# Kernel tuning notes

Measured on AMD Instinct MI355X. Metric: run time of the kernel, lower is better.

Reference implementation:

```python
import jax, jax.numpy as jnp
import numpy as np

NUM_ITER = 20
EPS = 1e-8


def _conv(x, w, pad):
    # x: [N, Cin, H, W], w: [Cout, Cin, kh, kw] (cross-correlation, like torch conv2d)
    return jax.lax.conv_general_dilated(
        x, w, window_strides=(1, 1), padding=pad,
        dimension_numbers=('NCHW', 'OIHW', 'NCHW'))


def setup_inputs() -> dict:
    key = jax.random.key(0)
    x = jax.random.normal(key, (2, 4, 3, 256, 256), dtype=jnp.float32)
    return {
        'x': x,
        'lam': jnp.array([0.02], dtype=jnp.float32),
        'tau': jnp.array([0.25], dtype=jnp.float32),
        'theta': jnp.array([0.1], dtype=jnp.float32),
        'wx': jnp.array([[-1.0, 1.0, 0.0]], dtype=jnp.float32),
        'wy': jnp.array([[-1.0], [1.0], [0.0]], dtype=jnp.float32),
    }


def reference(x, lam, tau, theta, wx, wy):
    # x: [2, B, C, H, W] -> pairs of single-channel images [NB, 2, H, W]
    F, B, C, H, W = x.shape
    NB = B * C
    xx = jnp.moveaxis(x.reshape(2, NB, H, W), 0, 1)  # [NB, 2, H, W]

    dt = x.dtype
    gx = jnp.array([[-1., 0., 1.], [-2., 0., 2.], [-1., 0., 1.]], dt) / 6.0
    gy = jnp.array([[-1., -2., -1.], [0., 0., 0.], [1., 2., 1.]], dt) / 6.0
    grad_w = jnp.stack([gx, gy])[:, None]          # [2,1,3,3] image gradient (fixed)
    gxu = jnp.array([[0., 0., 0.], [0., -1., 1.], [0., 0., 0.]], dt)
    gyu = jnp.array([[0., 0., 0.], [0., -1., 0.], [0., 1., 0.]], dt)
    grad_u_w = jnp.stack([gxu, gyu])[:, None]      # [2,1,3,3] flow gradient (fixed)
    wx_k = wx[None, None]                          # [1,1,1,3] trainable divergence stencil
    wy_k = wy[None, None]                          # [1,1,3,1]

    rho_c = (xx[:, 1] - xx[:, 0])[:, None]                       # [NB,1,H,W]
    grad_im = _conv(xx[:, 1:], grad_w, [(1, 1), (1, 1)])         # [NB,2,H,W]
    norm_grad = jnp.sum(grad_im * grad_im, axis=1, keepdims=True) + EPS

    u = jnp.zeros((NB, 2, H, W), dt)
    p1 = jnp.zeros((NB, 2, H, W), dt)
    p2 = jnp.zeros((NB, 2, H, W), dt)

    tl = theta * lam       # [1]
    tt = tau / theta       # [1]

    def div(p):  # p: [NB,2,H,W] -> [NB,1,H,W]
        return (_conv(p[:, 0:1], wx_k, [(0, 0), (1, 1)]) +
                _conv(p[:, 1:2], wy_k, [(1, 1), (0, 0)]))

    def body(carry, _):
        u, p1, p2 = carry
        rho = rho_c + jnp.sum(grad_im * u, axis=1, keepdims=True)
        th = tl * norm_grad
        v = u - jnp.where(jnp.abs(rho) < th,
                          rho * grad_im / norm_grad,
                          tl * grad_im * jnp.sign(rho))
        u0 = v[:, 0] + theta * div(p1)[:, 0]
        u1 = v[:, 1] + theta * div(p2)[:, 0]
        u = jnp.stack([u0, u1], axis=1)
        g1 = _conv(u[:, 0:1], grad_u_w, [(1, 1), (1, 1)])
        g2 = _conv(u[:, 1:2], grad_u_w, [(1, 1), (1, 1)])
        p1 = (p1 + tt * g1) / (1.0 + tt * jnp.sum(jnp.abs(g1), axis=1, keepdims=True))
        p2 = (p2 + tt * g2) / (1.0 + tt * jnp.sum(jnp.abs(g2), axis=1, keepdims=True))
        return (u, p1, p2), None

    (u, p1, p2), _ = jax.lax.scan(body, (u, p1, p2), None, length=NUM_ITER)
    return u.reshape(B, C, 2, H, W)
```

## Files before the change

kernel.cpp:

```cpp
#include <hip/hip_runtime.h>

#define W 256
#define H 256
#define HW (W*H)
#define NB 12
#define ROWS 16
#define BPI (H/ROWS)
#define NBLK (NB*BPI)
#define NTHREADS 1024
#define NUM_ITER 20
#define TVEPS 1e-8f
#define HPLANES 8
#define FLAG_MAGIC 0x5A170000


__device__ __forceinline__ float aload(const float* p) {
    return __hip_atomic_load(p, __ATOMIC_RELAXED, __HIP_MEMORY_SCOPE_AGENT);
}
__device__ __forceinline__ void astore(float* p, float v) {
    __hip_atomic_store(p, v, __ATOMIC_RELAXED, __HIP_MEMORY_SCOPE_AGENT);
}
__device__ __forceinline__ void waitflag(const int* f, int tgt) {
    while (__hip_atomic_load(f, __ATOMIC_RELAXED, __HIP_MEMORY_SCOPE_AGENT) != tgt)
        __builtin_amdgcn_s_sleep(1);
    asm volatile("" ::: "memory");
}
__device__ __forceinline__ void setflag(int* f, int tgt) {
    asm volatile("s_waitcnt vmcnt(0)" ::: "memory");
    __hip_atomic_store(f, tgt, __ATOMIC_RELAXED, __HIP_MEMORY_SCOPE_AGENT);
}
__device__ __forceinline__ float fastrcp(float x) { return __builtin_amdgcn_rcpf(x); }

#define LD4(dst, ptr) { const float4 _t = *reinterpret_cast<const float4*>(ptr); \
                        dst[0]=_t.x; dst[1]=_t.y; dst[2]=_t.z; dst[3]=_t.w; }
#define ST4(ptr, src) { float4 _t; _t.x=src[0]; _t.y=src[1]; _t.z=src[2]; _t.w=src[3]; \
                        *reinterpret_cast<float4*>(ptr) = _t; }

__global__ __launch_bounds__(NTHREADS, 1) void tvl1_ovl_kernel(
    const float* __restrict__ xin,
    const float* __restrict__ lam,
    const float* __restrict__ tau,
    const float* __restrict__ theta,
    const float* __restrict__ wxv,
    const float* __restrict__ wyv,
    float* __restrict__ uout,
    float* __restrict__ halo,
    int* __restrict__ flags)
{
    __shared__ float xu0[ROWS+1][W];
    __shared__ float xu1[ROWS+1][W];
    __shared__ float xq1[ROWS][W];
    __shared__ float xq2[ROWS][W];

    const int tid  = threadIdx.x;
    const int lane = tid & 63;
    const int wv   = tid >> 6;
    const int x0   = lane << 2;
    const int b    = blockIdx.x;
    const int n    = b / BPI, bi = b % BPI;
    const int r0   = bi * ROWS;
    const int grow = r0 + wv;
    const bool notTop = (bi > 0), notBot = (bi < BPI-1);

    const float th0 = theta[0];
    const float tl  = th0 * lam[0];
    const float tt  = tau[0] / th0;
    const float wx0 = wxv[0], wx1 = wxv[1], wx2 = wxv[2];
    const float wy0 = wyv[0], wy1 = wyv[1], wy2 = wyv[2];

    const float* __restrict__ I0 = xin + (size_t)n * HW;
    const float* __restrict__ I1 = xin + (size_t)(NB + n) * HW;

    auto grad4 = [&](int row, float* rr, float* ggx, float* ggy) {
        #pragma unroll
        for (int c = 0; c < 4; ++c) {
            const int xc = x0 + c;
            const int idx = row * W + xc;
            const bool xm = xc > 0, xp = xc < W-1, ym = row > 0, yp = row < H-1;
            float a00=0.f,a01=0.f,a02=0.f,a10=0.f,a12=0.f,a20=0.f,a21=0.f,a22=0.f;
            if (ym) { a01=I1[idx-W]; if (xm) a00=I1[idx-W-1]; if (xp) a02=I1[idx-W+1]; }
            if (xm) a10=I1[idx-1];
            if (xp) a12=I1[idx+1];
            if (yp) { a21=I1[idx+W]; if (xm) a20=I1[idx+W-1]; if (xp) a22=I1[idx+W+1]; }
            ggx[c] = ((a02-a00) + 2.f*(a12-a10) + (a22-a20)) * (1.f/6.f);
            ggy[c] = ((a20-a00) + 2.f*(a21-a01) + (a22-a02)) * (1.f/6.f);
            rr[c]  = I1[idx] - I0[idx];
        }
    };

    float rho[4], gxr[4], gyr[4];
    grad4(grow, rho, gxr, gyr);
    float rho16[4]={0,0,0,0}, gx16[4]={0,0,0,0}, gy16[4]={0,0,0,0};
    if (wv == 14 && notBot) grad4(r0 + ROWS, rho16, gx16, gy16);

    for (int k = tid; k < (ROWS+1)*W; k += NTHREADS) { (&xu0[0][0])[k]=0.f; (&xu1[0][0])[k]=0.f; }
    for (int k = tid; k < ROWS*W;     k += NTHREADS) { (&xq1[0][0])[k]=0.f; (&xq2[0][0])[k]=0.f; }
    float u0[4]={0,0,0,0}, u1[4]={0,0,0,0};
    float p1x[4]={0,0,0,0}, p1y[4]={0,0,0,0}, p2x[4]={0,0,0,0}, p2y[4]={0,0,0,0};
    __syncthreads();

    auto ustep_dym = [&](const float* rr, const float* ggx, const float* ggy,
                         const float* uu0, const float* uu1,
                         const float* x1, const float* q1c, const float* q1p,
                         const float* x2, const float* q2c, const float* q2p,
                         float* o0, float* o1) {
        float l1 = __shfl_up(x1[3],1), l2 = __shfl_up(x2[3],1);
        if (lane == 0) { l1 = 0.f; l2 = 0.f; }
        float r1 = __shfl_down(x1[0],1), r2 = __shfl_down(x2[0],1);
        if (lane == 63) { r1 = 0.f; r2 = 0.f; }
        const float x1m[4]={l1,x1[0],x1[1],x1[2]}, x1p[4]={x1[1],x1[2],x1[3],r1};
        const float x2m[4]={l2,x2[0],x2[1],x2[2]}, x2p[4]={x2[1],x2[2],x2[3],r2};
        #pragma unroll
        for (int c = 0; c < 4; ++c) {
            const float r  = rr[c] + ggx[c]*uu0[c] + ggy[c]*uu1[c];
            const float ng = ggx[c]*ggx[c] + ggy[c]*ggy[c] + TVEPS;
            const float f  = (fabsf(r) < tl*ng) ? (r * fastrcp(ng)) : copysignf(tl, r);
            const float d1 = wx0*x1m[c] + wx1*x1[c] + wx2*x1p[c] + wy1*q1c[c] + wy2*q1p[c];
            const float d2 = wx0*x2m[c] + wx1*x2[c] + wx2*x2p[c] + wy1*q2c[c] + wy2*q2p[c];
            o0[c] = (uu0[c] - f*ggx[c]) + th0*d1;
            o1[c] = (uu1[c] - f*ggy[c]) + th0*d2;
        }
    };
    auto ustep_dyp = [&](const float* rr, const float* ggx, const float* ggy,
                         const float* uu0, const float* uu1,
                         const float* x1, const float* q1m, const float* q1c,
                         const float* x2, const float* q2m, const float* q2c,
                         float* o0, float* o1) {
        float l1 = __shfl_up(x1[3],1), l2 = __shfl_up(x2[3],1);
        if (lane == 0) { l1 = 0.f; l2 = 0.f; }
        float r1 = __shfl_down(x1[0],1), r2 = __shfl_down(x2[0],1);
        if (lane == 63) { r1 = 0.f; r2 = 0.f; }
        const float x1m[4]={l1,x1[0],x1[1],x1[2]}, x1p[4]={x1[1],x1[2],x1[3],r1};
        const float x2m[4]={l2,x2[0],x2[1],x2[2]}, x2p[4]={x2[1],x2[2],x2[3],r2};
        #pragma unroll
        for (int c = 0; c < 4; ++c) {
            const float r  = rr[c] + ggx[c]*uu0[c] + ggy[c]*uu1[c];
            const float ng = ggx[c]*ggx[c] + ggy[c]*ggy[c] + TVEPS;
            const float f  = (fabsf(r) < tl*ng) ? (r * fastrcp(ng)) : copysignf(tl, r);
            const float d1 = wx0*x1m[c] + wx1*x1[c] + wx2*x1p[c] + wy0*q1m[c] + wy1*q1c[c];
            const float d2 = wx0*x2m[c] + wx1*x2[c] + wx2*x2p[c] + wy0*q2m[c] + wy1*q2c[c];
            o0[c] = (uu0[c] - f*ggx[c]) + th0*d1;
            o1[c] = (uu1[c] - f*ggy[c]) + th0*d2;
        }
    };
    auto ustepF = [&](const float* q1m, const float* q1p, const float* q2m, const float* q2p) {
        float l1 = __shfl_up(p1x[3],1), l2 = __shfl_up(p2x[3],1);
        if (lane == 0) { l1 = 0.f; l2 = 0.f; }
        float r1 = __shfl_down(p1x[0],1), r2 = __shfl_down(p2x[0],1);
        if (lane == 63) { r1 = 0.f; r2 = 0.f; }
        const float x1m[4]={l1,p1x[0],p1x[1],p1x[2]}, x1p[4]={p1x[1],p1x[2],p1x[3],r1};
        const float x2m[4]={l2,p2x[0],p2x[1],p2x[2]}, x2p[4]={p2x[1],p2x[2],p2x[3],r2};
        #pragma unroll
        for (int c = 0; c < 4; ++c) {
            const float r  = rho[c] + gxr[c]*u0[c] + gyr[c]*u1[c];
            const float ng = gxr[c]*gxr[c] + gyr[c]*gyr[c] + TVEPS;
            const float f  = (fabsf(r) < tl*ng) ? (r * fastrcp(ng)) : copysignf(tl, r);
            const float d1 = wx0*x1m[c] + wx1*p1x[c] + wx2*x1p[c]
                           + wy0*q1m[c] + wy1*p1y[c] + wy2*q1p[c];
            const float d2 = wx0*x2m[c] + wx1*p2x[c] + wx2*x2p[c]
                           + wy0*q2m[c] + wy1*p2y[c] + wy2*q2p[c];
            u0[c] = (u0[c] - f*gxr[c]) + th0*d1;
            u1[c] = (u1[c] - f*gyr[c]) + th0*d2;
        }
    };

    for (int it = 0; it < NUM_ITER; ++it) {
        const bool last = (it == NUM_ITER-1);

        if (wv == 0) {
            float pyp1[4], pyp2[4];
            LD4(pyp1, &xq1[1][x0]); LD4(pyp2, &xq2[1][x0]);
            float o0[4], o1[4];
            ustep_dym(rho, gxr, gyr, u0, u1, p1x, p1y, pyp1, p2x, p2y, pyp2, o0, o1);
            float hym1[4]={0,0,0,0}, hym2[4]={0,0,0,0};
            if (it > 0 && notTop) {
                if (lane == 0) waitflag(&flags[(size_t)(it-1)*3*NBLK + 2*NBLK + (b-1)],
                                        FLAG_MAGIC | (it-1));
                const float* hp = halo + ((size_t)(it-1)*NBLK + (b-1))*HPLANES*W;
                #pragma unroll
                for (int c = 0; c < 4; ++c) {
                    hym1[c] = aload(hp + 6*W + x0 + c);
                    hym2[c] = aload(hp + 7*W + x0 + c);
                }
            }
            #pragma unroll
            for (int c = 0; c < 4; ++c) {
                u0[c] = o0[c] + th0*(wy0*hym1[c]);
                u1[c] = o1[c] + th0*(wy0*hym2[c]);
            }
        } else if (wv == ROWS-1) {
            float pym1[4], pym2[4];
            LD4(pym1, &xq1[ROWS-2][x0]); LD4(pym2, &xq2[ROWS-2][x0]);
            float o0[4], o1[4];
            ustep_dyp(rho, gxr, gyr, u0, u1, p1x, pym1, p1y, p2x, pym2, p2y, o0, o1);
            float hyp1[4]={0,0,0,0}, hyp2[4]={0,0,0,0};
            if (it > 0 && notBot) {
                if (lane == 0) waitflag(&flags[(size_t)(it-1)*3*NBLK + 0*NBLK + (b+1)],
                                        FLAG_MAGIC | (it-1));
                const float* hp = halo + ((size_t)(it-1)*NBLK + (b+1))*HPLANES*W;
                #pragma unroll
                for (int c = 0; c < 4; ++c) {
                    hyp1[c] = aload(hp + 1*W + x0 + c);
                    hyp2[c] = aload(hp + 3*W + x0 + c);
                }
            }
            #pragma unroll
            for (int c = 0; c < 4; ++c) {
                u0[c] = o0[c] + th0*(wy2*hyp1[c]);
                u1[c] = o1[c] + th0*(wy2*hyp2[c]);
            }
        } else {
            float pym1[4], pym2[4], pyp1[4], pyp2[4];
            LD4(pym1, &xq1[wv-1][x0]); LD4(pym2, &xq2[wv-1][x0]);
            LD4(pyp1, &xq1[wv+1][x0]); LD4(pyp2, &xq2[wv+1][x0]);
            ustepF(pym1, pyp1, pym2, pyp2);
        }

        if (last) {
            float* __restrict__ o0 = uout + (size_t)(2*n)   * HW + (size_t)grow * W + x0;
            float* __restrict__ o1 = uout + (size_t)(2*n+1) * HW + (size_t)grow * W + x0;
            ST4(o0, u0); ST4(o1, u1);
            break;
        }
        ST4(&xu0[wv][x0], u0); ST4(&xu1[wv][x0], u1);

        if (wv == 14 && notBot) {
            float c16x1[4]={0,0,0,0}, c16x2[4]={0,0,0,0};
            float c16c1[4]={0,0,0,0}, c16c2[4]={0,0,0,0};
            float c16p1[4]={0,0,0,0}, c16p2[4]={0,0,0,0};
            if (it > 0) {
                int* fb = flags + (size_t)(it-1)*3*NBLK;
                if (lane < 2) waitflag(&fb[lane*NBLK + (b+1)], FLAG_MAGIC | (it-1));
                const float* hp = halo + ((size_t)(it-1)*NBLK + (b+1))*HPLANES*W;
                #pragma unroll
                for (int c = 0; c < 4; ++c) {
                    c16x1[c] = aload(hp + 0*W + x0 + c);
                    c16c1[c] = aload(hp + 1*W + x0 + c);
                    c16x2[c] = aload(hp + 2*W + x0 + c);
                    c16c2[c] = aload(hp + 3*W + x0 + c);
                    c16p1[c] = aload(hp + 4*W + x0 + c);
                    c16p2[c] = aload(hp + 5*W + x0 + c);
                }
            }
            float q115[4], q215[4], u160[4], u161[4];
            LD4(q115, &xq1[ROWS-1][x0]); LD4(q215, &xq2[ROWS-1][x0]);
            LD4(u160, &xu0[ROWS][x0]);   LD4(u161, &xu1[ROWS][x0]);
            float n160[4], n161[4];
            ustep_dym(rho16, gx16, gy16, u160, u161,
                      c16x1, c16c1, c16p1, c16x2, c16c2, c16p2, n160, n161);
            #pragma unroll
            for (int c = 0; c < 4; ++c) {
                n160[c] += th0*(wy0*q115[c]);
                n161[c] += th0*(wy0*q215[c]);
            }
            ST4(&xu0[ROWS][x0], n160); ST4(&xu1[ROWS][x0], n161);
        }
        __syncthreads();

        float uy0[4], uy1[4];
        if (grow == H-1) { for (int c=0;c<4;++c){ uy0[c]=0.f; uy1[c]=0.f; } }
        else             { LD4(uy0, &xu0[wv+1][x0]); LD4(uy1, &xu1[wv+1][x0]); }
        float ur0 = __shfl_down(u0[0], 1), ur1 = __shfl_down(u1[0], 1);
        if (lane == 63) { ur0 = 0.f; ur1 = 0.f; }
        #pragma unroll
        for (int c = 0; c < 4; ++c) {
            const float uxp0 = (c < 3) ? u0[c+1] : ur0;
            const float uxp1 = (c < 3) ? u1[c+1] : ur1;
            const float g1x = uxp0 - u0[c];
            const float g1y = uy0[c] - u0[c];
            const float g2x = uxp1 - u1[c];
            const float g2y = uy1[c] - u1[c];
            const float rc1 = fastrcp(1.f + tt * (fabsf(g1x) + fabsf(g1y)));
            const float rc2 = fastrcp(1.f + tt * (fabsf(g2x) + fabsf(g2y)));
            p1x[c] = (p1x[c] + tt*g1x) * rc1;
            p1y[c] = (p1y[c] + tt*g1y) * rc1;
            p2x[c] = (p2x[c] + tt*g2x) * rc2;
            p2y[c] = (p2y[c] + tt*g2y) * rc2;
        }
        ST4(&xq1[wv][x0], p1y); ST4(&xq2[wv][x0], p2y);

        {
            float* hw = halo + ((size_t)it * NBLK + b) * HPLANES * W;
            int* fw = flags + (size_t)it * 3 * NBLK;
            const int ft = FLAG_MAGIC | it;
            if (wv == 0 && notTop) {
                #pragma unroll
                for (int c = 0; c < 4; ++c) {
                    astore(hw + 0*W + x0 + c, p1x[c]);
                    astore(hw + 1*W + x0 + c, p1y[c]);
                    astore(hw + 2*W + x0 + c, p2x[c]);
                    astore(hw + 3*W + x0 + c, p2y[c]);
                }
                if (lane == 0) setflag(&fw[0*NBLK + b], ft);
            } else if (wv == 1 && notTop) {
                #pragma unroll
                for (int c = 0; c < 4; ++c) {
                    astore(hw + 4*W + x0 + c, p1y[c]);
                    astore(hw + 5*W + x0 + c, p2y[c]);
                }
                if (lane == 0) setflag(&fw[1*NBLK + b], ft);
            } else if (wv == ROWS-1 && notBot) {
                #pragma unroll
                for (int c = 0; c < 4; ++c) {
                    astore(hw + 6*W + x0 + c, p1y[c]);
                    astore(hw + 7*W + x0 + c, p2y[c]);
                }
                if (lane == 0) setflag(&fw[2*NBLK + b], ft);
            }
        }
        __syncthreads();
    }
}


__global__ void precompute_kernel(const float* __restrict__ x,
                                  float* __restrict__ u,
                                  float* __restrict__ ws) {
    const int row = blockIdx.x;
    const int n = row / H, y = row % H;
    const int xx = threadIdx.x;
    const int idx = y * W + xx;
    const float* __restrict__ I0 = x + (size_t)n * HW;
    const float* __restrict__ I1 = x + (size_t)(NB + n) * HW;
    float* __restrict__ p1  = ws;
    float* __restrict__ p2  = ws + (size_t)2 * NB * HW;
    float* __restrict__ rho = ws + (size_t)4 * NB * HW;
    float* __restrict__ gxp = ws + (size_t)5 * NB * HW;
    float* __restrict__ gyp = ws + (size_t)6 * NB * HW;
    const float i1c = I1[idx];
    const bool xm = xx > 0, xp = xx < W - 1, ym = y > 0, yp = y < H - 1;
    float a00=0.f,a01=0.f,a02=0.f,a10=0.f,a12=0.f,a20=0.f,a21=0.f,a22=0.f;
    if (ym) { a01 = I1[idx-W]; if (xm) a00 = I1[idx-W-1]; if (xp) a02 = I1[idx-W+1]; }
    if (xm) a10 = I1[idx-1];
    if (xp) a12 = I1[idx+1];
    if (yp) { a21 = I1[idx+W]; if (xm) a20 = I1[idx+W-1]; if (xp) a22 = I1[idx+W+1]; }
    const float gxv = ((a02-a00) + 2.f*(a12-a10) + (a22-a20)) * (1.f/6.f);
    const float gyv = ((a20-a00) + 2.f*(a21-a01) + (a22-a02)) * (1.f/6.f);
    const size_t np = (size_t)n * HW;
    rho[np+idx] = i1c - I0[idx];
    gxp[np+idx] = gxv;
    gyp[np+idx] = gyv;
    u[(size_t)(2*n)*HW + idx] = 0.f;   u[(size_t)(2*n+1)*HW + idx] = 0.f;
    p1[(size_t)(2*n)*HW + idx] = 0.f;  p1[(size_t)(2*n+1)*HW + idx] = 0.f;
    p2[(size_t)(2*n)*HW + idx] = 0.f;  p2[(size_t)(2*n+1)*HW + idx] = 0.f;
}

__global__ void u_kernel(const float* __restrict__ ws,
                         float* __restrict__ u,
                         const float* __restrict__ lam,
                         const float* __restrict__ theta,
                         const float* __restrict__ wxv,
                         const float* __restrict__ wyv) {
    const int row = blockIdx.x;
    const int n = row / H, y = row % H;
    const int xx = threadIdx.x;
    const int idx = y * W + xx;
    const size_t np = (size_t)n * HW;
    const float* __restrict__ p1  = ws;
    const float* __restrict__ p2  = ws + (size_t)2 * NB * HW;
    const float* __restrict__ rho_c = ws + (size_t)4 * NB * HW;
    const float* __restrict__ gxp = ws + (size_t)5 * NB * HW;
    const float* __restrict__ gyp = ws + (size_t)6 * NB * HW;
    const float th0 = theta[0];
    const float tl = th0 * lam[0];
    const float wx0 = wxv[0], wx1 = wxv[1], wx2 = wxv[2];
    const float wy0 = wyv[0], wy1 = wyv[1], wy2 = wyv[2];
    const float gx = gxp[np+idx];
    const float gy = gyp[np+idx];
    float* __restrict__ u0p = u + (size_t)(2*n)*HW;
    float* __restrict__ u1p = u + (size_t)(2*n+1)*HW;
    const float u0 = u0p[idx], u1 = u1p[idx];
    const float rho = rho_c[np+idx] + gx*u0 + gy*u1;
    const float ng = gx*gx + gy*gy + TVEPS;
    const float th = tl * ng;
    float s0, s1;
    if (fabsf(rho) < th) { const float d = rho/ng; s0 = d*gx; s1 = d*gy; }
    else { const float sg = (rho > 0.f) ? 1.f : ((rho < 0.f) ? -1.f : 0.f);
           s0 = tl*gx*sg; s1 = tl*gy*sg; }
    const float v0 = u0 - s0, v1 = u1 - s1;
    const float* __restrict__ p1xp = p1 + (size_t)(2*n)*HW;
    const float* __restrict__ p1yp = p1 + (size_t)(2*n+1)*HW;
    const float* __restrict__ p2xp = p2 + (size_t)(2*n)*HW;
    const float* __restrict__ p2yp = p2 + (size_t)(2*n+1)*HW;
    float d1 = wx1*p1xp[idx] + wy1*p1yp[idx];
    float d2 = wx1*p2xp[idx] + wy1*p2yp[idx];
    if (xx > 0)     { d1 += wx0*p1xp[idx-1]; d2 += wx0*p2xp[idx-1]; }
    if (xx < W-1)   { d1 += wx2*p1xp[idx+1]; d2 += wx2*p2xp[idx+1]; }
    if (y > 0)      { d1 += wy0*p1yp[idx-W]; d2 += wy0*p2yp[idx-W]; }
    if (y < H-1)    { d1 += wy2*p1yp[idx+W]; d2 += wy2*p2yp[idx+W]; }
    u0p[idx] = v0 + th0*d1;
    u1p[idx] = v1 + th0*d2;
}

__global__ void p_kernel(const float* __restrict__ u,
                         float* __restrict__ ws,
                         const float* __restrict__ tau,
                         const float* __restrict__ theta) {
    const int row = blockIdx.x;
    const int n = row / H, y = row % H;
    const int xx = threadIdx.x;
    const int idx = y * W + xx;
    float* __restrict__ p1 = ws;
    float* __restrict__ p2 = ws + (size_t)2 * NB * HW;
    const float tt = tau[0] / theta[0];
    const float* __restrict__ u0p = u + (size_t)(2*n)*HW;
    const float* __restrict__ u1p = u + (size_t)(2*n+1)*HW;
    const float c0 = u0p[idx];
    const float g1x = ((xx < W-1) ? u0p[idx+1] : 0.f) - c0;
    const float g1y = ((y < H-1) ? u0p[idx+W] : 0.f) - c0;
    const float c1 = u1p[idx];
    const float g2x = ((xx < W-1) ? u1p[idx+1] : 0.f) - c1;
    const float g2y = ((y < H-1) ? u1p[idx+W] : 0.f) - c1;
    float* __restrict__ p1xp = p1 + (size_t)(2*n)*HW;
    float* __restrict__ p1yp = p1 + (size_t)(2*n+1)*HW;
    float* __restrict__ p2xp = p2 + (size_t)(2*n)*HW;
    float* __restrict__ p2yp = p2 + (size_t)(2*n+1)*HW;
    const float den1 = 1.f + tt * (fabsf(g1x) + fabsf(g1y));
    p1xp[idx] = (p1xp[idx] + tt*g1x) / den1;
    p1yp[idx] = (p1yp[idx] + tt*g1y) / den1;
    const float den2 = 1.f + tt * (fabsf(g2x) + fabsf(g2y));
    p2xp[idx] = (p2xp[idx] + tt*g2x) / den2;
    p2yp[idx] = (p2yp[idx] + tt*g2y) / den2;
}

extern "C" void kernel_launch(void* const* d_in, const int* in_sizes, int n_in,
                              void* d_out, int out_size, void* d_ws, size_t ws_size,
                              hipStream_t stream) {
    const float* x     = (const float*)d_in[0];
    const float* lam   = (const float*)d_in[1];
    const float* tau   = (const float*)d_in[2];
    const float* theta = (const float*)d_in[3];
    const float* wxv   = (const float*)d_in[4];
    const float* wyv   = (const float*)d_in[5];
    float* u = (float*)d_out;

    const size_t halo_floats = (size_t)(NUM_ITER-1) * NBLK * HPLANES * W;
    const size_t need = halo_floats * sizeof(float)
                      + (size_t)(NUM_ITER-1) * 3 * NBLK * sizeof(int);

    if (ws_size >= need) {
        float* halo = (float*)d_ws;
        int* flags = (int*)((char*)d_ws + halo_floats * sizeof(float));
        void* args[] = { (void*)&x, (void*)&lam, (void*)&tau, (void*)&theta,
                         (void*)&wxv, (void*)&wyv, (void*)&u, (void*)&halo, (void*)&flags };
        hipLaunchCooperativeKernel((void*)tvl1_ovl_kernel, dim3(NBLK), dim3(NTHREADS),
                                   args, 0, stream);
    } else {
        float* ws = (float*)d_ws;
        const dim3 grid(NB * H);
        const dim3 block(W);
        precompute_kernel<<<grid, block, 0, stream>>>(x, u, ws);
        for (int it = 0; it < NUM_ITER; ++it) {
            u_kernel<<<grid, block, 0, stream>>>(ws, u, lam, theta, wxv, wyv);
            p_kernel<<<grid, block, 0, stream>>>(u, ws, tau, theta);
        }
    }
}
```

Baseline: 111.3 us.

## Defer cross-block halo waits past local u-step and use LDS flags for boundary rows

Restructures each iteration so boundary waves run their local u-update first and only wait on neighbour halo data after the workgroup barrier, folding the halo contribution in later. Flag stores for the previous iteration's halo are deferred to the start of the next iteration so the memory waitcnt overlaps other work. Wave 14 keeps its recomputed ghost row in registers and exchanges boundary rows with wave 15 through LDS flags instead of an extra barrier. This aims to hide inter-block spin-wait latency, at the cost of more complex ordering and possible subtle sync bugs.

```diff
diff --git a/kernel.cpp b/kernel.cpp
--- a/kernel.cpp
+++ b/kernel.cpp
@@ -29,6 +29,12 @@
     asm volatile("s_waitcnt vmcnt(0)" ::: "memory");
     __hip_atomic_store(f, tgt, __ATOMIC_RELAXED, __HIP_MEMORY_SCOPE_AGENT);
 }
+__device__ __forceinline__ void lset(int* f, int v) {
+    __hip_atomic_store(f, v, __ATOMIC_RELEASE, __HIP_MEMORY_SCOPE_WORKGROUP);
+}
+__device__ __forceinline__ void lwait(int* f, int v) {
+    while (__hip_atomic_load(f, __ATOMIC_ACQUIRE, __HIP_MEMORY_SCOPE_WORKGROUP) < v) {}
+}
 __device__ __forceinline__ float fastrcp(float x) { return __builtin_amdgcn_rcpf(x); }
 
 #define LD4(dst, ptr) { const float4 _t = *reinterpret_cast<const float4*>(ptr); \
@@ -36,7 +42,7 @@
 #define ST4(ptr, src) { float4 _t; _t.x=src[0]; _t.y=src[1]; _t.z=src[2]; _t.w=src[3]; \
                         *reinterpret_cast<float4*>(ptr) = _t; }
 
-__global__ __launch_bounds__(NTHREADS, 1) void tvl1_ovl_kernel(
+__global__ __launch_bounds__(NTHREADS, 1) void tvl1_pb_kernel(
     const float* __restrict__ xin,
     const float* __restrict__ lam,
     const float* __restrict__ tau,
@@ -51,6 +57,7 @@
     __shared__ float xu1[ROWS+1][W];
     __shared__ float xq1[ROWS][W];
     __shared__ float xq2[ROWS][W];
+    __shared__ int   sF[2];
 
     const int tid  = threadIdx.x;
     const int lane = tid & 63;
@@ -91,10 +98,12 @@
     float rho[4], gxr[4], gyr[4];
     grad4(grow, rho, gxr, gyr);
     float rho16[4]={0,0,0,0}, gx16[4]={0,0,0,0}, gy16[4]={0,0,0,0};
+    float u16_0[4]={0,0,0,0}, u16_1[4]={0,0,0,0};
     if (wv == 14 && notBot) grad4(r0 + ROWS, rho16, gx16, gy16);
 
     for (int k = tid; k < (ROWS+1)*W; k += NTHREADS) { (&xu0[0][0])[k]=0.f; (&xu1[0][0])[k]=0.f; }
     for (int k = tid; k < ROWS*W;     k += NTHREADS) { (&xq1[0][0])[k]=0.f; (&xq2[0][0])[k]=0.f; }
+    if (tid == 0) { sF[0] = 0; sF[1] = 0; }
     float u0[4]={0,0,0,0}, u1[4]={0,0,0,0};
     float p1x[4]={0,0,0,0}, p1y[4]={0,0,0,0}, p2x[4]={0,0,0,0}, p2y[4]={0,0,0,0};
     __syncthreads();
@@ -163,113 +172,15 @@
             u1[c] = (u1[c] - f*gyr[c]) + th0*d2;
         }
     };
-
-    for (int it = 0; it < NUM_ITER; ++it) {
-        const bool last = (it == NUM_ITER-1);
-
-        if (wv == 0) {
-            float pyp1[4], pyp2[4];
-            LD4(pyp1, &xq1[1][x0]); LD4(pyp2, &xq2[1][x0]);
-            float o0[4], o1[4];
-            ustep_dym(rho, gxr, gyr, u0, u1, p1x, p1y, pyp1, p2x, p2y, pyp2, o0, o1);
-            float hym1[4]={0,0,0,0}, hym2[4]={0,0,0,0};
-            if (it > 0 && notTop) {
-                if (lane == 0) waitflag(&flags[(size_t)(it-1)*3*NBLK + 2*NBLK + (b-1)],
-                                        FLAG_MAGIC | (it-1));
-                const float* hp = halo + ((size_t)(it-1)*NBLK + (b-1))*HPLANES*W;
-                #pragma unroll
-                for (int c = 0; c < 4; ++c) {
-                    hym1[c] = aload(hp + 6*W + x0 + c);
-                    hym2[c] = aload(hp + 7*W + x0 + c);
-                }
-            }
-            #pragma unroll
-            for (int c = 0; c < 4; ++c) {
-                u0[c] = o0[c] + th0*(wy0*hym1[c]);
-                u1[c] = o1[c] + th0*(wy0*hym2[c]);
-            }
-        } else if (wv == ROWS-1) {
-            float pym1[4], pym2[4];
-            LD4(pym1, &xq1[ROWS-2][x0]); LD4(pym2, &xq2[ROWS-2][x0]);
-            float o0[4], o1[4];
-            ustep_dyp(rho, gxr, gyr, u0, u1, p1x, pym1, p1y, p2x, pym2, p2y, o0, o1);
-            float hyp1[4]={0,0,0,0}, hyp2[4]={0,0,0,0};
-            if (it > 0 && notBot) {
-                if (lane == 0) waitflag(&flags[(size_t)(it-1)*3*NBLK + 0*NBLK + (b+1)],
-                                        FLAG_MAGIC | (it-1));
-                const float* hp = halo + ((size_t)(it-1)*NBLK + (b+1))*HPLANES*W;
-                #pragma unroll
-                for (int c = 0; c < 4; ++c) {
-                    hyp1[c] = aload(hp + 1*W + x0 + c);
-                    hyp2[c] = aload(hp + 3*W + x0 + c);
-                }
-            }
-            #pragma unroll
-            for (int c = 0; c < 4; ++c) {
-                u0[c] = o0[c] + th0*(wy2*hyp1[c]);
-                u1[c] = o1[c] + th0*(wy2*hyp2[c]);
-            }
-        } else {
-            float pym1[4], pym2[4], pyp1[4], pyp2[4];
-            LD4(pym1, &xq1[wv-1][x0]); LD4(pym2, &xq2[wv-1][x0]);
-            LD4(pyp1, &xq1[wv+1][x0]); LD4(pyp2, &xq2[wv+1][x0]);
-            ustepF(pym1, pyp1, pym2, pyp2);
-        }
-
-        if (last) {
-            float* __restrict__ o0 = uout + (size_t)(2*n)   * HW + (size_t)grow * W + x0;
-            float* __restrict__ o1 = uout + (size_t)(2*n+1) * HW + (size_t)grow * W + x0;
-            ST4(o0, u0); ST4(o1, u1);
-            break;
-        }
-        ST4(&xu0[wv][x0], u0); ST4(&xu1[wv][x0], u1);
-
-        if (wv == 14 && notBot) {
-            float c16x1[4]={0,0,0,0}, c16x2[4]={0,0,0,0};
-            float c16c1[4]={0,0,0,0}, c16c2[4]={0,0,0,0};
-            float c16p1[4]={0,0,0,0}, c16p2[4]={0,0,0,0};
-            if (it > 0) {
-                int* fb = flags + (size_t)(it-1)*3*NBLK;
-                if (lane < 2) waitflag(&fb[lane*NBLK + (b+1)], FLAG_MAGIC | (it-1));
-                const float* hp = halo + ((size_t)(it-1)*NBLK + (b+1))*HPLANES*W;
-                #pragma unroll
-                for (int c = 0; c < 4; ++c) {
-                    c16x1[c] = aload(hp + 0*W + x0 + c);
-                    c16c1[c] = aload(hp + 1*W + x0 + c);
-                    c16x2[c] = aload(hp + 2*W + x0 + c);
-                    c16c2[c] = aload(hp + 3*W + x0 + c);
-                    c16p1[c] = aload(hp + 4*W + x0 + c);
-                    c16p2[c] = aload(hp + 5*W + x0 + c);
-                }
-            }
-            float q115[4], q215[4], u160[4], u161[4];
-            LD4(q115, &xq1[ROWS-1][x0]); LD4(q215, &xq2[ROWS-1][x0]);
-            LD4(u160, &xu0[ROWS][x0]);   LD4(u161, &xu1[ROWS][x0]);
-            float n160[4], n161[4];
-            ustep_dym(rho16, gx16, gy16, u160, u161,
-                      c16x1, c16c1, c16p1, c16x2, c16c2, c16p2, n160, n161);
-            #pragma unroll
-            for (int c = 0; c < 4; ++c) {
-                n160[c] += th0*(wy0*q115[c]);
-                n161[c] += th0*(wy0*q215[c]);
-            }
-            ST4(&xu0[ROWS][x0], n160); ST4(&xu1[ROWS][x0], n161);
-        }
-        __syncthreads();
-
-        float uy0[4], uy1[4];
-        if (grow == H-1) { for (int c=0;c<4;++c){ uy0[c]=0.f; uy1[c]=0.f; } }
-        else             { LD4(uy0, &xu0[wv+1][x0]); LD4(uy1, &xu1[wv+1][x0]); }
-        float ur0 = __shfl_down(u0[0], 1), ur1 = __shfl_down(u1[0], 1);
+    auto pstep = [&](const float* uy0, const float* uy1) {
+        float ur0 = __shfl_down(u0[0],1), ur1 = __shfl_down(u1[0],1);
         if (lane == 63) { ur0 = 0.f; ur1 = 0.f; }
         #pragma unroll
         for (int c = 0; c < 4; ++c) {
             const float uxp0 = (c < 3) ? u0[c+1] : ur0;
             const float uxp1 = (c < 3) ? u1[c+1] : ur1;
-            const float g1x = uxp0 - u0[c];
-            const float g1y = uy0[c] - u0[c];
-            const float g2x = uxp1 - u1[c];
-            const float g2y = uy1[c] - u1[c];
+            const float g1x = uxp0 - u0[c], g1y = uy0[c] - u0[c];
+            const float g2x = uxp1 - u1[c], g2y = uy1[c] - u1[c];
             const float rc1 = fastrcp(1.f + tt * (fabsf(g1x) + fabsf(g1y)));
             const float rc2 = fastrcp(1.f + tt * (fabsf(g2x) + fabsf(g2y)));
             p1x[c] = (p1x[c] + tt*g1x) * rc1;
@@ -277,13 +188,115 @@
             p2x[c] = (p2x[c] + tt*g2x) * rc2;
             p2y[c] = (p2y[c] + tt*g2y) * rc2;
         }
-        ST4(&xq1[wv][x0], p1y); ST4(&xq2[wv][x0], p2y);
-
-        {
-            float* hw = halo + ((size_t)it * NBLK + b) * HPLANES * W;
-            int* fw = flags + (size_t)it * 3 * NBLK;
-            const int ft = FLAG_MAGIC | it;
-            if (wv == 0 && notTop) {
+    };
+
+    for (int it = 0; it < NUM_ITER; ++it) {
+        const bool last = (it == NUM_ITER-1);
+        const int fseq = it + 1;
+
+        if (it > 0 && lane == 0) {
+            int* fw = flags + (size_t)(it-1) * 3 * NBLK;
+            const int ft = FLAG_MAGIC | (it-1);
+            if (wv == 0 && notTop)           setflag(&fw[0*NBLK + b], ft);
+            else if (wv == 1 && notTop)      setflag(&fw[1*NBLK + b], ft);
+            else if (wv == ROWS-1 && notBot) setflag(&fw[2*NBLK + b], ft);
+        }
+
+        if (wv == 0) {
+            float pyp1v[4], pyp2v[4];
+            LD4(pyp1v, &xq1[1][x0]); LD4(pyp2v, &xq2[1][x0]);
+            float o0[4], o1[4];
+            ustep_dym(rho, gxr, gyr, u0, u1, p1x, p1y, pyp1v, p2x, p2y, pyp2v, o0, o1);
+            if (last) {
+                float hym1[4]={0,0,0,0}, hym2[4]={0,0,0,0};
+                if (it > 0 && notTop) {
+                    if (lane == 0) waitflag(&flags[(size_t)(it-1)*3*NBLK + 2*NBLK + (b-1)],
+                                            FLAG_MAGIC | (it-1));
+                    const float* hp = halo + ((size_t)(it-1)*NBLK + (b-1))*HPLANES*W;
+                    #pragma unroll
+                    for (int c = 0; c < 4; ++c) {
+                        hym1[c] = aload(hp + 6*W + x0 + c);
+                        hym2[c] = aload(hp + 7*W + x0 + c);
+                    }
+                }
+                #pragma unroll
+                for (int c = 0; c < 4; ++c) {
+                    u0[c] = o0[c] + th0*(wy0*hym1[c]);
+                    u1[c] = o1[c] + th0*(wy0*hym2[c]);
+                }
+            } else {
+                #pragma unroll
+                for (int c = 0; c < 4; ++c) { u0[c] = o0[c]; u1[c] = o1[c]; }
+            }
+        } else if (wv == ROWS-1) {
+            float pym1v[4], pym2v[4];
+            LD4(pym1v, &xq1[ROWS-2][x0]); LD4(pym2v, &xq2[ROWS-2][x0]);
+            float o0[4], o1[4];
+            ustep_dyp(rho, gxr, gyr, u0, u1, p1x, pym1v, p1y, p2x, pym2v, p2y, o0, o1);
+            if (last) {
+                float hyp1[4]={0,0,0,0}, hyp2[4]={0,0,0,0};
+                if (it > 0 && notBot) {
+                    if (lane == 0) waitflag(&flags[(size_t)(it-1)*3*NBLK + 0*NBLK + (b+1)],
+                                            FLAG_MAGIC | (it-1));
+                    const float* hp = halo + ((size_t)(it-1)*NBLK + (b+1))*HPLANES*W;
+                    #pragma unroll
+                    for (int c = 0; c < 4; ++c) {
+                        hyp1[c] = aload(hp + 1*W + x0 + c);
+                        hyp2[c] = aload(hp + 3*W + x0 + c);
+                    }
+                }
+                #pragma unroll
+                for (int c = 0; c < 4; ++c) {
+                    u0[c] = o0[c] + th0*(wy2*hyp1[c]);
+                    u1[c] = o1[c] + th0*(wy2*hyp2[c]);
+                }
+            } else {
+                #pragma unroll
+                for (int c = 0; c < 4; ++c) { u0[c] = o0[c]; u1[c] = o1[c]; }
+            }
+        } else {
+            float pym1v[4], pym2v[4], pyp1v[4], pyp2v[4];
+            LD4(pym1v, &xq1[wv-1][x0]); LD4(pym2v, &xq2[wv-1][x0]);
+            LD4(pyp1v, &xq1[wv+1][x0]); LD4(pyp2v, &xq2[wv+1][x0]);
+            ustepF(pym1v, pyp1v, pym2v, pyp2v);
+        }
+        float q115[4], q215[4];
+        if (wv == 14 && notBot && !last) {
+            LD4(q115, &xq1[ROWS-1][x0]); LD4(q215, &xq2[ROWS-1][x0]);
+        }
+
+        if (last) {
+            float* __restrict__ o0p = uout + (size_t)(2*n)   * HW + (size_t)grow * W + x0;
+            float* __restrict__ o1p = uout + (size_t)(2*n+1) * HW + (size_t)grow * W + x0;
+            ST4(o0p, u0); ST4(o1p, u1);
+            break;
+        }
+        if (wv >= 1 && wv <= 14) { ST4(&xu0[wv][x0], u0); ST4(&xu1[wv][x0], u1); }
+        __syncthreads();
+
+        if (wv == 0) {
+            float hym1[4]={0,0,0,0}, hym2[4]={0,0,0,0};
+            if (it > 0 && notTop) {
+                if (lane == 0) waitflag(&flags[(size_t)(it-1)*3*NBLK + 2*NBLK + (b-1)],
+                                        FLAG_MAGIC | (it-1));
+                const float* hp = halo + ((size_t)(it-1)*NBLK + (b-1))*HPLANES*W;
+                #pragma unroll
+                for (int c = 0; c < 4; ++c) {
+                    hym1[c] = aload(hp + 6*W + x0 + c);
+                    hym2[c] = aload(hp + 7*W + x0 + c);
+                }
+            }
+            #pragma unroll
+            for (int c = 0; c < 4; ++c) {
+                u0[c] += th0*(wy0*hym1[c]);
+                u1[c] += th0*(wy0*hym2[c]);
+            }
+            float uy0[4], uy1[4];
+            LD4(uy0, &xu0[1][x0]); LD4(uy1, &xu1[1][x0]);
+            pstep(uy0, uy1);
+            ST4(&xq1[0][x0], p1y); ST4(&xq2[0][x0], p2y);
+            if (notTop) {
+                float* hw = halo + ((size_t)it * NBLK + b) * HPLANES * W;
                 #pragma unroll
                 for (int c = 0; c < 4; ++c) {
                     astore(hw + 0*W + x0 + c, p1x[c]);
@@ -291,21 +304,85 @@
                     astore(hw + 2*W + x0 + c, p2x[c]);
                     astore(hw + 3*W + x0 + c, p2y[c]);
                 }
-                if (lane == 0) setflag(&fw[0*NBLK + b], ft);
-            } else if (wv == 1 && notTop) {
+            }
+        } else if (wv == ROWS-1) {
+            float hyp1[4]={0,0,0,0}, hyp2[4]={0,0,0,0};
+            if (it > 0 && notBot) {
+                if (lane == 0) waitflag(&flags[(size_t)(it-1)*3*NBLK + 0*NBLK + (b+1)],
+                                        FLAG_MAGIC | (it-1));
+                const float* hp = halo + ((size_t)(it-1)*NBLK + (b+1))*HPLANES*W;
+                #pragma unroll
+                for (int c = 0; c < 4; ++c) {
+                    hyp1[c] = aload(hp + 1*W + x0 + c);
+                    hyp2[c] = aload(hp + 3*W + x0 + c);
+                }
+            }
+            #pragma unroll
+            for (int c = 0; c < 4; ++c) {
+                u0[c] += th0*(wy2*hyp1[c]);
+                u1[c] += th0*(wy2*hyp2[c]);
+            }
+            ST4(&xu0[ROWS-1][x0], u0); ST4(&xu1[ROWS-1][x0], u1);
+            lset(&sF[0], fseq);
+            float uy0[4], uy1[4];
+            if (grow == H-1) { for (int c=0;c<4;++c){ uy0[c]=0.f; uy1[c]=0.f; } }
+            else { lwait(&sF[1], fseq); LD4(uy0, &xu0[ROWS][x0]); LD4(uy1, &xu1[ROWS][x0]); }
+            pstep(uy0, uy1);
+            ST4(&xq1[ROWS-1][x0], p1y); ST4(&xq2[ROWS-1][x0], p2y);
+            if (notBot) {
+                float* hw = halo + ((size_t)it * NBLK + b) * HPLANES * W;
+                #pragma unroll
+                for (int c = 0; c < 4; ++c) {
+                    astore(hw + 6*W + x0 + c, p1y[c]);
+                    astore(hw + 7*W + x0 + c, p2y[c]);
+                }
+            }
+        } else if (wv == 14) {
+            if (notBot) {
+                float pl0[4]={0,0,0,0}, pl1[4]={0,0,0,0}, pl2[4]={0,0,0,0};
+                float pl3[4]={0,0,0,0}, pl4[4]={0,0,0,0}, pl5[4]={0,0,0,0};
+                if (it > 0) {
+                    int* fb = flags + (size_t)(it-1)*3*NBLK;
+                    if (lane < 2) waitflag(&fb[lane*NBLK + (b+1)], FLAG_MAGIC | (it-1));
+                    const float* hp = halo + ((size_t)(it-1)*NBLK + (b+1))*HPLANES*W;
+                    #pragma unroll
+                    for (int c = 0; c < 4; ++c) {
+                        pl0[c] = aload(hp + 0*W + x0 + c);
+                        pl1[c] = aload(hp + 1*W + x0 + c);
+                        pl2[c] = aload(hp + 2*W + x0 + c);
+                        pl3[c] = aload(hp + 3*W + x0 + c);
+                        pl4[c] = aload(hp + 4*W + x0 + c);
+                        pl5[c] = aload(hp + 5*W + x0 + c);
+                    }
+                }
+                float n0[4], n1[4];
+                ustep_dym(rho16, gx16, gy16, u16_0, u16_1,
+                          pl0, pl1, pl4, pl2, pl3, pl5, n0, n1);
+                #pragma unroll
+                for (int c = 0; c < 4; ++c) {
+                    u16_0[c] = n0[c] + th0*(wy0*q115[c]);
+                    u16_1[c] = n1[c] + th0*(wy0*q215[c]);
+                }
+                ST4(&xu0[ROWS][x0], u16_0); ST4(&xu1[ROWS][x0], u16_1);
+                lset(&sF[1], fseq);
+            }
+            lwait(&sF[0], fseq);
+            float uy0[4], uy1[4];
+            LD4(uy0, &xu0[ROWS-1][x0]); LD4(uy1, &xu1[ROWS-1][x0]);
+            pstep(uy0, uy1);
+            ST4(&xq1[14][x0], p1y); ST4(&xq2[14][x0], p2y);
+        } else {
+            float uy0[4], uy1[4];
+            LD4(uy0, &xu0[wv+1][x0]); LD4(uy1, &xu1[wv+1][x0]);
+            pstep(uy0, uy1);
+            ST4(&xq1[wv][x0], p1y); ST4(&xq2[wv][x0], p2y);
+            if (wv == 1 && notTop) {
+                float* hw = halo + ((size_t)it * NBLK + b) * HPLANES * W;
                 #pragma unroll
                 for (int c = 0; c < 4; ++c) {
                     astore(hw + 4*W + x0 + c, p1y[c]);
                     astore(hw + 5*W + x0 + c, p2y[c]);
                 }
-                if (lane == 0) setflag(&fw[1*NBLK + b], ft);
-            } else if (wv == ROWS-1 && notBot) {
-                #pragma unroll
-                for (int c = 0; c < 4; ++c) {
-                    astore(hw + 6*W + x0 + c, p1y[c]);
-                    astore(hw + 7*W + x0 + c, p2y[c]);
-                }
-                if (lane == 0) setflag(&fw[2*NBLK + b], ft);
             }
         }
         __syncthreads();
@@ -443,7 +520,7 @@
         int* flags = (int*)((char*)d_ws + halo_floats * sizeof(float));
         void* args[] = { (void*)&x, (void*)&lam, (void*)&tau, (void*)&theta,
                          (void*)&wxv, (void*)&wyv, (void*)&u, (void*)&halo, (void*)&flags };
-        hipLaunchCooperativeKernel((void*)tvl1_ovl_kernel, dim3(NBLK), dim3(NTHREADS),
+        hipLaunchCooperativeKernel((void*)tvl1_pb_kernel, dim3(NBLK), dim3(NTHREADS),
                                    args, 0, stream);
     } else {
         float* ws = (float*)d_ws;
```

Result: slower. 119.8 us (+7.6%).

## Defer halo flag publication past barrier and opportunistically prefetch neighbor halos

Applied to the files above, without the earlier changes.

Halo-ready flags are no longer set right after the halo stores. They are set at the start of the next iteration, after the block barrier, which removes the vmcnt(0) drain from the critical path before __syncthreads. Boundary waves now peek at the neighbor's flag before their own u-step. If it is already set, they load the halo rows early to overlap latency, and they fall back to the blocking wait only when it is not. The risk is that flag publication is delayed by up to one barrier, which could lengthen neighbors' waits, and correctness relies on relaxed atomic ordering.

```diff
diff --git a/kernel.cpp b/kernel.cpp
--- a/kernel.cpp
+++ b/kernel.cpp
@@ -25,6 +25,9 @@
         __builtin_amdgcn_s_sleep(1);
     asm volatile("" ::: "memory");
 }
+__device__ __forceinline__ int peekflag(const int* f) {
+    return __hip_atomic_load(f, __ATOMIC_RELAXED, __HIP_MEMORY_SCOPE_AGENT);
+}
 __device__ __forceinline__ void setflag(int* f, int tgt) {
     asm volatile("s_waitcnt vmcnt(0)" ::: "memory");
     __hip_atomic_store(f, tgt, __ATOMIC_RELAXED, __HIP_MEMORY_SCOPE_AGENT);
@@ -36,7 +39,7 @@
 #define ST4(ptr, src) { float4 _t; _t.x=src[0]; _t.y=src[1]; _t.z=src[2]; _t.w=src[3]; \
                         *reinterpret_cast<float4*>(ptr) = _t; }
 
-__global__ __launch_bounds__(NTHREADS, 1) void tvl1_ovl_kernel(
+__global__ __launch_bounds__(NTHREADS, 1) void tvl1_opp_kernel(
     const float* __restrict__ xin,
     const float* __restrict__ lam,
     const float* __restrict__ tau,
@@ -166,17 +169,36 @@
 
     for (int it = 0; it < NUM_ITER; ++it) {
         const bool last = (it == NUM_ITER-1);
+        const int tgt = FLAG_MAGIC | (it-1);
+
+        if (it > 0 && lane == 0) {
+            int* fw = flags + (size_t)(it-1) * 3 * NBLK;
+            if (wv == 0 && notTop)           setflag(&fw[0*NBLK + b], tgt);
+            else if (wv == 1 && notTop)      setflag(&fw[1*NBLK + b], tgt);
+            else if (wv == ROWS-1 && notBot) setflag(&fw[2*NBLK + b], tgt);
+        }
 
         if (wv == 0) {
+            bool rdy = false;
+            float hym1[4]={0,0,0,0}, hym2[4]={0,0,0,0};
+            const float* hp = halo + ((size_t)(it-1)*NBLK + (b-1))*HPLANES*W;
+            if (it > 0 && notTop) {
+                rdy = (peekflag(&flags[(size_t)(it-1)*3*NBLK + 2*NBLK + (b-1)]) == tgt);
+                asm volatile("" ::: "memory");
+                if (rdy) {
+                    #pragma unroll
+                    for (int c = 0; c < 4; ++c) {
+                        hym1[c] = aload(hp + 6*W + x0 + c);
+                        hym2[c] = aload(hp + 7*W + x0 + c);
+                    }
+                }
+            }
             float pyp1[4], pyp2[4];
             LD4(pyp1, &xq1[1][x0]); LD4(pyp2, &xq2[1][x0]);
             float o0[4], o1[4];
             ustep_dym(rho, gxr, gyr, u0, u1, p1x, p1y, pyp1, p2x, p2y, pyp2, o0, o1);
-            float hym1[4]={0,0,0,0}, hym2[4]={0,0,0,0};
-            if (it > 0 && notTop) {
-                if (lane == 0) waitflag(&flags[(size_t)(it-1)*3*NBLK + 2*NBLK + (b-1)],
-                                        FLAG_MAGIC | (it-1));
-                const float* hp = halo + ((size_t)(it-1)*NBLK + (b-1))*HPLANES*W;
+            if (it > 0 && notTop && !rdy) {
+                if (lane == 0) waitflag(&flags[(size_t)(it-1)*3*NBLK + 2*NBLK + (b-1)], tgt);
                 #pragma unroll
                 for (int c = 0; c < 4; ++c) {
                     hym1[c] = aload(hp + 6*W + x0 + c);
@@ -189,15 +211,26 @@
                 u1[c] = o1[c] + th0*(wy0*hym2[c]);
             }
         } else if (wv == ROWS-1) {
+            bool rdy = false;
+            float hyp1[4]={0,0,0,0}, hyp2[4]={0,0,0,0};
+            const float* hp = halo + ((size_t)(it-1)*NBLK + (b+1))*HPLANES*W;
+            if (it > 0 && notBot) {
+                rdy = (peekflag(&flags[(size_t)(it-1)*3*NBLK + 0*NBLK + (b+1)]) == tgt);
+                asm volatile("" ::: "memory");
+                if (rdy) {
+                    #pragma unroll
+                    for (int c = 0; c < 4; ++c) {
+                        hyp1[c] = aload(hp + 1*W + x0 + c);
+                        hyp2[c] = aload(hp + 3*W + x0 + c);
+                    }
+                }
+            }
             float pym1[4], pym2[4];
             LD4(pym1, &xq1[ROWS-2][x0]); LD4(pym2, &xq2[ROWS-2][x0]);
             float o0[4], o1[4];
             ustep_dyp(rho, gxr, gyr, u0, u1, p1x, pym1, p1y, p2x, pym2, p2y, o0, o1);
-            float hyp1[4]={0,0,0,0}, hyp2[4]={0,0,0,0};
-            if (it > 0 && notBot) {
-                if (lane == 0) waitflag(&flags[(size_t)(it-1)*3*NBLK + 0*NBLK + (b+1)],
-                                        FLAG_MAGIC | (it-1));
-                const float* hp = halo + ((size_t)(it-1)*NBLK + (b+1))*HPLANES*W;
+            if (it > 0 && notBot && !rdy) {
+                if (lane == 0) waitflag(&flags[(size_t)(it-1)*3*NBLK + 0*NBLK + (b+1)], tgt);
                 #pragma unroll
                 for (int c = 0; c < 4; ++c) {
                     hyp1[c] = aload(hp + 1*W + x0 + c);
@@ -230,8 +263,13 @@
             float c16p1[4]={0,0,0,0}, c16p2[4]={0,0,0,0};
             if (it > 0) {
                 int* fb = flags + (size_t)(it-1)*3*NBLK;
-                if (lane < 2) waitflag(&fb[lane*NBLK + (b+1)], FLAG_MAGIC | (it-1));
                 const float* hp = halo + ((size_t)(it-1)*NBLK + (b+1))*HPLANES*W;
+                const bool rdy = (peekflag(&fb[0*NBLK + (b+1)]) == tgt) &&
+                                 (peekflag(&fb[1*NBLK + (b+1)]) == tgt);
+                asm volatile("" ::: "memory");
+                if (!rdy) {
+                    if (lane < 2) waitflag(&fb[lane*NBLK + (b+1)], tgt);
+                }
                 #pragma unroll
                 for (int c = 0; c < 4; ++c) {
                     c16x1[c] = aload(hp + 0*W + x0 + c);
@@ -281,8 +319,6 @@
 
         {
             float* hw = halo + ((size_t)it * NBLK + b) * HPLANES * W;
-            int* fw = flags + (size_t)it * 3 * NBLK;
-            const int ft = FLAG_MAGIC | it;
             if (wv == 0 && notTop) {
                 #pragma unroll
                 for (int c = 0; c < 4; ++c) {
@@ -291,21 +327,18 @@
                     astore(hw + 2*W + x0 + c, p2x[c]);
                     astore(hw + 3*W + x0 + c, p2y[c]);
                 }
-                if (lane == 0) setflag(&fw[0*NBLK + b], ft);
             } else if (wv == 1 && notTop) {
                 #pragma unroll
                 for (int c = 0; c < 4; ++c) {
                     astore(hw + 4*W + x0 + c, p1y[c]);
                     astore(hw + 5*W + x0 + c, p2y[c]);
                 }
-                if (lane == 0) setflag(&fw[1*NBLK + b], ft);
             } else if (wv == ROWS-1 && notBot) {
                 #pragma unroll
                 for (int c = 0; c < 4; ++c) {
                     astore(hw + 6*W + x0 + c, p1y[c]);
                     astore(hw + 7*W + x0 + c, p2y[c]);
                 }
-                if (lane == 0) setflag(&fw[2*NBLK + b], ft);
             }
         }
         __syncthreads();
@@ -443,7 +476,7 @@
         int* flags = (int*)((char*)d_ws + halo_floats * sizeof(float));
         void* args[] = { (void*)&x, (void*)&lam, (void*)&tau, (void*)&theta,
                          (void*)&wxv, (void*)&wyv, (void*)&u, (void*)&halo, (void*)&flags };
-        hipLaunchCooperativeKernel((void*)tvl1_ovl_kernel, dim3(NBLK), dim3(NTHREADS),
+        hipLaunchCooperativeKernel((void*)tvl1_opp_kernel, dim3(NBLK), dim3(NTHREADS),
                                    args, 0, stream);
     } else {
         float* ws = (float*)d_ws;
```

After: 102.2 us, median of 2. 1.09x faster.
